# Performance work log

Measured on AMD Instinct MI355X. Metric: run time of the kernel, lower is better.

The kernel has to match this reference:

```python
import jax, jax.numpy as jnp
import numpy as np

N, E, R, H = 50000, 400000, 3, 3
IN, HID, OUT, C, B = 128, 64, 64, 16, 8


def _deg_norm(idx):
    # DGL GraphConv norm='both': deg.clamp(min=1) ** -0.5
    deg = jax.ops.segment_sum(jnp.ones(idx.shape, jnp.float32), idx, N)
    return jnp.maximum(deg, 1.0) ** -0.5


def _graph_conv(h, W, b, s, d):
    # h: [N, ..., F_in]; norm by src out-degree, matmul, scatter-sum to dst, norm by dst in-degree
    ns, nd = _deg_norm(s), _deg_norm(d)
    bshape = (N,) + (1,) * (h.ndim - 1)
    hw = (h * ns.reshape(bshape)) @ W
    agg = jax.ops.segment_sum(hw[s], d, N)
    return agg * nd.reshape(bshape) + b


def _gat(h, W, al, ar, b, s, d):
    # h: [N, HID] -> [N, H, HID] multi-head GAT with edge softmax over incoming edges
    f = (h @ W).reshape(N, H, HID)
    el = jnp.sum(f * al, axis=-1)  # [N, H]
    er = jnp.sum(f * ar, axis=-1)  # [N, H]
    e = jax.nn.leaky_relu(el[s] + er[d], 0.2)  # [E, H]
    m = jax.ops.segment_max(e, d, N)
    ez = jnp.exp(e - m[d])
    z = jax.ops.segment_sum(ez, d, N)
    alpha = ez / (z[d] + 1e-9)  # [E, H]
    out = jax.ops.segment_sum(alpha[:, :, None] * f[s], d, N)  # [N, H, HID]
    return out + b.reshape(H, HID)


def setup_inputs() -> dict:
    key = jax.random.key(0)
    k = jax.random.split(key, 12)
    s = 0.05
    return {
        "x": jax.random.normal(k[0], (N, IN), jnp.float32),
        "src": jax.random.randint(k[1], (R, E), 0, N, jnp.int32),
        "dst": jax.random.randint(k[2], (R, E), 0, N, jnp.int32),
        "graph_id": (jnp.arange(N, dtype=jnp.int32) * B // N).astype(jnp.int32),
        "W1": jax.random.normal(k[3], (R, IN, HID), jnp.float32) * s,
        "b1": jnp.zeros((R, HID), jnp.float32),
        "Wg": jax.random.normal(k[4], (R, HID, H * HID), jnp.float32) * s,
        "al": jax.random.normal(k[5], (R, H, HID), jnp.float32) * s,
        "ar": jax.random.normal(k[6], (R, H, HID), jnp.float32) * s,
        "bg": jnp.zeros((R, H * HID), jnp.float32),
        "W2": jax.random.normal(k[7], (R, HID, OUT), jnp.float32) * s,
        "b2": jnp.zeros((R, OUT), jnp.float32),
        "Wc": jax.random.normal(k[8], (OUT, C), jnp.float32) * s,
        "bc": jnp.zeros((C,), jnp.float32),
    }


def reference(x, src, dst, graph_id, W1, b1, Wg, al, ar, bg, W2, b2, Wc, bc):
    # conv1: per-relation GraphConv, aggregate='sum'
    h = sum(_graph_conv(x, W1[r], b1[r], src[r], dst[r]) for r in range(R))  # [N, HID]
    # F.normalize (L2 over dim=1, eps=1e-12)
    h = h / jnp.maximum(jnp.linalg.norm(h, axis=1, keepdims=True), 1e-12)
    # gatconv: per-relation GAT (3 heads), aggregate='sum'
    h = sum(_gat(h, Wg[r], al[r], ar[r], bg[r], src[r], dst[r]) for r in range(R))  # [N, H, HID]
    h = jax.nn.relu(h)
    # dropout(0.3) omitted: deterministic eval reference
    # conv2: GraphConv applied per head
    h = sum(_graph_conv(h, W2[r], b2[r], src[r], dst[r]) for r in range(R))  # [N, H, OUT]
    h = jax.nn.sigmoid(h)
    # dgl.mean_nodes over batched graphs
    cnt = jax.ops.segment_sum(jnp.ones((N,), jnp.float32), graph_id, B)
    pooled = jax.ops.segment_sum(h, graph_id, B) / jnp.maximum(cnt, 1.0)[:, None, None]  # [B, H, OUT]
    hg = jax.nn.sigmoid(pooled @ Wc + bc)  # [B, H, C]
    return jnp.mean(hg, axis=2)  # [B, H]
```

## Files before the change

kernel.cpp:

```cpp
#include <hip/hip_runtime.h>
#include <math.h>

#define NN 50000
#define EE 400000
#define RR 3
#define NH 3
#define FIN 128
#define HID 64
#define FOUT 64
#define NC 16
#define NB 8
#define NGAT 208

typedef __attribute__((ext_vector_type(8))) short v8s;
typedef __attribute__((ext_vector_type(4))) float v4f;
typedef unsigned short u16;
typedef __attribute__((ext_vector_type(4))) unsigned short u16x4;

__device__ __forceinline__ u16 f2b(float f) {
  unsigned u = __float_as_uint(f);
  return (u16)((u + 0x7fffu + ((u >> 16) & 1u)) >> 16);
}
__device__ __forceinline__ float b2f(u16 b) {
  return __uint_as_float(((unsigned)b) << 16);
}
__device__ __forceinline__ float wexp(float e) {
  e = e > 0.f ? e : 0.2f * e;
  return __expf(e);
}

__global__ void k_deg(const int* __restrict__ src, const int* __restrict__ dst,
                      int* __restrict__ degs, int* __restrict__ degd) {
  int i = blockIdx.x * 256 + threadIdx.x;
  if (i >= RR * EE) return;
  int r = i / EE;
  atomicAdd(&degs[r * NN + src[i]], 1);
  atomicAdd(&degd[r * NN + dst[i]], 1);
}

__global__ void k_norm(const int* __restrict__ degs, const int* __restrict__ degd,
                       float* __restrict__ ns, float* __restrict__ nd) {
  int i = blockIdx.x * 256 + threadIdx.x;
  if (i >= RR * NN) return;
  ns[i] = 1.0f / sqrtf((float)(degs[i] > 1 ? degs[i] : 1));
  nd[i] = 1.0f / sqrtf((float)(degd[i] > 1 ? degd[i] : 1));
}

__global__ void k_scan1(const int* __restrict__ deg, int* __restrict__ offs,
                        int* __restrict__ bsum) {
  __shared__ int sh[256];
  int gid = blockIdx.x * 256 + threadIdx.x;
  int v = (gid < RR * NN) ? deg[gid] : 0;
  sh[threadIdx.x] = v;
  __syncthreads();
  for (int off = 1; off < 256; off <<= 1) {
    int t = (threadIdx.x >= off) ? sh[threadIdx.x - off] : 0;
    __syncthreads();
    sh[threadIdx.x] += t;
    __syncthreads();
  }
  if (gid < RR * NN) offs[gid] = sh[threadIdx.x] - v;
  if (threadIdx.x == 255) bsum[blockIdx.x] = sh[255];
}

__global__ void k_scan2(int* __restrict__ bsum, int nb) {
  __shared__ int sh[1024];
  int v = (threadIdx.x < nb) ? bsum[threadIdx.x] : 0;
  sh[threadIdx.x] = v;
  __syncthreads();
  for (int off = 1; off < 1024; off <<= 1) {
    int t = (threadIdx.x >= off) ? sh[threadIdx.x - off] : 0;
    __syncthreads();
    sh[threadIdx.x] += t;
    __syncthreads();
  }
  if (threadIdx.x < nb) bsum[threadIdx.x] = sh[threadIdx.x] - v;
}

__global__ void k_scan3(int* __restrict__ offs, const int* __restrict__ bsum,
                        int* __restrict__ cursor) {
  int i = blockIdx.x * 256 + threadIdx.x;
  if (i >= RR * NN) return;
  int v = offs[i] + bsum[i / 256];
  offs[i] = v;
  cursor[i] = v;
}

__global__ void k_fill(const int* __restrict__ src, const int* __restrict__ dst,
                       int* __restrict__ cursor, int* __restrict__ esrc,
                       int* __restrict__ edst) {
  int i = blockIdx.x * 256 + threadIdx.x;
  if (i >= RR * EE) return;
  int r = i / EE;
  int d = dst[i];
  int pos = atomicAdd(&cursor[r * NN + d], 1);
  esrc[pos] = src[i];
  edst[pos] = d;
}

__global__ void k_cast(const float4* __restrict__ in, u16x4* __restrict__ out, int n4) {
  int i = blockIdx.x * 256 + threadIdx.x;
  if (i >= n4) return;
  float4 v = in[i];
  u16x4 o;
  o.x = f2b(v.x); o.y = f2b(v.y); o.z = f2b(v.z); o.w = f2b(v.w);
  out[i] = o;
}

__global__ void k_bcomp(const float* __restrict__ Wg, const float* __restrict__ al,
                        const float* __restrict__ ar, float* __restrict__ B) {
  int i = blockIdx.x * 256 + threadIdx.x;
  if (i >= RR * HID * NGAT) return;
  int col = i % NGAT;
  int k = (i / NGAT) % HID;
  int r = i / (NGAT * HID);
  float v = 0.f;
  if (col < NH * HID) {
    v = Wg[((size_t)(r * HID + k)) * (NH * HID) + col];
  } else if (col < NH * HID + 6) {
    int c2 = col - NH * HID;
    int isar = c2 / NH, h = c2 % NH;
    const float* wg = Wg + ((size_t)(r * HID + k)) * (NH * HID) + h * HID;
    const float* av = (isar ? ar : al) + (r * NH + h) * HID;
    float a = 0.f;
#pragma unroll 8
    for (int c = 0; c < HID; ++c) a += wg[c] * av[c];
    v = a;
  }
  B[i] = v;
}

template <int K, int N, int SCALE_MODE>
__global__ __launch_bounds__(256) void k_gemm(const u16* __restrict__ A,
                                              const float* __restrict__ B0, int bstr,
                                              u16* __restrict__ C0, long cstr,
                                              const float* __restrict__ s0, int sstr,
                                              int M) {
  constexpr int KP = K + 8;
  __shared__ __align__(16) u16 Bt[N * KP];
  const float* B = B0 + (size_t)blockIdx.y * bstr;
  u16* C = C0 + (size_t)blockIdx.y * cstr;
  const float* scale = s0 + (size_t)blockIdx.y * sstr;
  for (int i = threadIdx.x; i < K * N; i += 256) {
    int k = i / N, n = i % N;
    Bt[n * KP + k] = f2b(B[(size_t)k * N + n]);
  }
  __syncthreads();
  int wid = threadIdx.x >> 6, lane = threadIdx.x & 63;
  int l15 = lane & 15, lg = lane >> 4;
  constexpr int NT = N / 16;
  int ntiles = (M + 63) >> 6;
  for (int tile = blockIdx.x; tile < ntiles; tile += gridDim.x) {
    int mbase = tile * 64 + wid * 16;
    v4f acc[NT];
#pragma unroll
    for (int t = 0; t < NT; ++t) acc[t] = (v4f)(0.f);
    int arow = mbase + l15;
    if (arow >= M) arow = M - 1;
    const u16* ap = A + (size_t)arow * K + lg * 8;
#pragma unroll
    for (int ks = 0; ks < K / 32; ++ks) {
      v8s a = *(const v8s*)(ap + ks * 32);
#pragma unroll
      for (int t = 0; t < NT; ++t) {
        v8s b = *(const v8s*)(&Bt[(t * 16 + l15) * KP + lg * 8 + ks * 32]);
        acc[t] = __builtin_amdgcn_mfma_f32_16x16x32_bf16(a, b, acc[t], 0, 0, 0);
      }
    }
#pragma unroll
    for (int q = 0; q < 4; ++q) {
      int row = mbase + lg * 4 + q;
      if (row < M) {
        float s = 1.f;
        if (SCALE_MODE == 1) s = scale[row];
        if (SCALE_MODE == 2) s = scale[row / NH];
#pragma unroll
        for (int t = 0; t < NT; ++t)
          C[(size_t)row * N + t * 16 + l15] = f2b(acc[t][q] * s);
      }
    }
  }
}

__global__ void k_g1(const int* __restrict__ offs, const int* __restrict__ degd,
                     const int* __restrict__ esrc, const u16* __restrict__ hw,
                     const float* __restrict__ nd, const float* __restrict__ b1,
                     u16* __restrict__ h1b) {
  int node = blockIdx.x * 4 + (threadIdx.x >> 6);
  int lane = threadIdx.x & 63;
  if (node >= NN) return;
  float v = 0.f;
#pragma unroll
  for (int r = 0; r < RR; ++r) {
    int start = offs[r * NN + node];
    int deg = degd[r * NN + node];
    const u16* base = hw + (size_t)r * NN * HID + lane;
    float t = 0.f;
    int j = 0;
    for (; j + 4 <= deg; j += 4) {
      int s0 = esrc[start + j], s1 = esrc[start + j + 1];
      int s2 = esrc[start + j + 2], s3 = esrc[start + j + 3];
      float a0 = b2f(base[(size_t)s0 * HID]);
      float a1 = b2f(base[(size_t)s1 * HID]);
      float a2 = b2f(base[(size_t)s2 * HID]);
      float a3 = b2f(base[(size_t)s3 * HID]);
      t += (a0 + a1) + (a2 + a3);
    }
    for (; j < deg; ++j) t += b2f(base[(size_t)esrc[start + j] * HID]);
    v += t * nd[r * NN + node];
  }
  v += b1[lane] + b1[HID + lane] + b1[2 * HID + lane];
  float sq = v * v;
  for (int off = 32; off; off >>= 1) sq += __shfl_xor(sq, off);
  float nrm = sqrtf(sq);
  nrm = nrm > 1e-12f ? nrm : 1e-12f;
  h1b[node * HID + lane] = f2b(v / nrm);
}

__global__ void k_elx(const u16* __restrict__ fb, u16* __restrict__ elr) {
  int i = blockIdx.x * 256 + threadIdx.x;
  if (i >= RR * NN) return;
  const u16* row = fb + (size_t)i * NGAT + NH * HID;
  u16x4 a, b;
  a.x = row[0]; a.y = row[1]; a.z = row[2]; a.w = 0;
  b.x = row[3]; b.y = row[4]; b.z = row[5]; b.w = 0;
  *(u16x4*)(elr + (size_t)i * 8) = a;
  *(u16x4*)(elr + (size_t)i * 8 + 4) = b;
}

__global__ void k_ew(const int* __restrict__ esrc, const int* __restrict__ edst,
                     const u16* __restrict__ elr, u16* __restrict__ ew) {
  int i = blockIdx.x * 256 + threadIdx.x;
  if (i >= RR * EE) return;
  int r = i / EE;
  int s = esrc[i], d = edst[i];
  const u16* es = elr + ((size_t)(r * NN + s)) * 8;
  const u16* ed = elr + ((size_t)(r * NN + d)) * 8 + 4;
  u16x4 o;
  o.x = f2b(wexp(b2f(es[0]) + b2f(ed[0])));
  o.y = f2b(wexp(b2f(es[1]) + b2f(ed[1])));
  o.z = f2b(wexp(b2f(es[2]) + b2f(ed[2])));
  o.w = 0;
  *(u16x4*)(ew + (size_t)i * 4) = o;
}

__global__ void k_gatg(const int* __restrict__ offs, const int* __restrict__ degd,
                       const int* __restrict__ esrc, const u16* __restrict__ fb,
                       const u16* __restrict__ ew, const float* __restrict__ bg,
                       u16* __restrict__ gatb) {
  int node = blockIdx.x * 4 + (threadIdx.x >> 6);
  int lane = threadIdx.x & 63;
  if (node >= NN) return;
  float o0 = 0.f, o1 = 0.f, o2 = 0.f;
#pragma unroll
  for (int r = 0; r < RR; ++r) {
    const u16* f = fb + (size_t)r * NN * NGAT + lane;
    int start = offs[r * NN + node];
    int deg = degd[r * NN + node];
    float z0 = 0.f, z1 = 0.f, z2 = 0.f;
    float a0 = 0.f, a1 = 0.f, a2 = 0.f;
    int j = 0;
    for (; j + 4 <= deg; j += 4) {
      int p = start + j;
      int s0 = esrc[p], s1 = esrc[p + 1], s2 = esrc[p + 2], s3 = esrc[p + 3];
      u16x4 wa = *(const u16x4*)(ew + (size_t)p * 4);
      u16x4 wb = *(const u16x4*)(ew + (size_t)(p + 1) * 4);
      u16x4 wc = *(const u16x4*)(ew + (size_t)(p + 2) * 4);
      u16x4 wd = *(const u16x4*)(ew + (size_t)(p + 3) * 4);
      const u16* q0 = f + (size_t)s0 * NGAT;
      const u16* q1 = f + (size_t)s1 * NGAT;
      const u16* q2 = f + (size_t)s2 * NGAT;
      const u16* q3 = f + (size_t)s3 * NGAT;
      float w;
      w = b2f(wa.x); z0 += w; a0 += w * b2f(q0[0]);
      w = b2f(wa.y); z1 += w; a1 += w * b2f(q0[HID]);
      w = b2f(wa.z); z2 += w; a2 += w * b2f(q0[2 * HID]);
      w = b2f(wb.x); z0 += w; a0 += w * b2f(q1[0]);
      w = b2f(wb.y); z1 += w; a1 += w * b2f(q1[HID]);
      w = b2f(wb.z); z2 += w; a2 += w * b2f(q1[2 * HID]);
      w = b2f(wc.x); z0 += w; a0 += w * b2f(q2[0]);
      w = b2f(wc.y); z1 += w; a1 += w * b2f(q2[HID]);
      w = b2f(wc.z); z2 += w; a2 += w * b2f(q2[2 * HID]);
      w = b2f(wd.x); z0 += w; a0 += w * b2f(q3[0]);
      w = b2f(wd.y); z1 += w; a1 += w * b2f(q3[HID]);
      w = b2f(wd.z); z2 += w; a2 += w * b2f(q3[2 * HID]);
    }
    for (; j < deg; ++j) {
      int p = start + j;
      int s0 = esrc[p];
      u16x4 wa = *(const u16x4*)(ew + (size_t)p * 4);
      const u16* q0 = f + (size_t)s0 * NGAT;
      float w;
      w = b2f(wa.x); z0 += w; a0 += w * b2f(q0[0]);
      w = b2f(wa.y); z1 += w; a1 += w * b2f(q0[HID]);
      w = b2f(wa.z); z2 += w; a2 += w * b2f(q0[2 * HID]);
    }
    o0 += a0 / (z0 + 1e-9f);
    o1 += a1 / (z1 + 1e-9f);
    o2 += a2 / (z2 + 1e-9f);
  }
  float ov[NH] = {o0, o1, o2};
#pragma unroll
  for (int h = 0; h < NH; ++h) {
    int j = h * HID + lane;
    float v = ov[h] + bg[j] + bg[NH * HID + j] + bg[2 * NH * HID + j];
    gatb[(size_t)node * (NH * HID) + j] = f2b(fmaxf(v, 0.f));
  }
}

__global__ void k_g2(const int* __restrict__ offs, const int* __restrict__ degd,
                     const int* __restrict__ esrc, const u16* __restrict__ fb,
                     const float* __restrict__ nd, const float* __restrict__ b2,
                     u16* __restrict__ agg2b) {
  int node = blockIdx.x * 4 + (threadIdx.x >> 6);
  int lane = threadIdx.x & 63;
  if (node >= NN) return;
  float o0 = 0.f, o1 = 0.f, o2 = 0.f;
#pragma unroll
  for (int r = 0; r < RR; ++r) {
    const u16* hw = fb + (size_t)r * NN * NH * FOUT + lane;
    int start = offs[r * NN + node];
    int deg = degd[r * NN + node];
    float a0 = 0.f, a1 = 0.f, a2 = 0.f;
    int j = 0;
    for (; j + 4 <= deg; j += 4) {
      int p = start + j;
      const u16* q0 = hw + (size_t)esrc[p] * (NH * FOUT);
      const u16* q1 = hw + (size_t)esrc[p + 1] * (NH * FOUT);
      const u16* q2 = hw + (size_t)esrc[p + 2] * (NH * FOUT);
      const u16* q3 = hw + (size_t)esrc[p + 3] * (NH * FOUT);
      a0 += (b2f(q0[0]) + b2f(q1[0])) + (b2f(q2[0]) + b2f(q3[0]));
      a1 += (b2f(q0[FOUT]) + b2f(q1[FOUT])) + (b2f(q2[FOUT]) + b2f(q3[FOUT]));
      a2 += (b2f(q0[2 * FOUT]) + b2f(q1[2 * FOUT])) +
            (b2f(q2[2 * FOUT]) + b2f(q3[2 * FOUT]));
    }
    for (; j < deg; ++j) {
      const u16* q0 = hw + (size_t)esrc[start + j] * (NH * FOUT);
      a0 += b2f(q0[0]);
      a1 += b2f(q0[FOUT]);
      a2 += b2f(q0[2 * FOUT]);
    }
    float ndv = nd[r * NN + node];
    o0 += a0 * ndv; o1 += a1 * ndv; o2 += a2 * ndv;
  }
  float b2s = b2[lane] + b2[FOUT + lane] + b2[2 * FOUT + lane];
  float ov[NH] = {o0, o1, o2};
#pragma unroll
  for (int h = 0; h < NH; ++h) {
    float v = 1.0f / (1.0f + __expf(-(ov[h] + b2s)));
    agg2b[(size_t)node * (NH * FOUT) + h * FOUT + lane] = f2b(v);
  }
}

__global__ void k_cnt2(const int* __restrict__ gid, float* __restrict__ cnt) {
  __shared__ int loc[NB];
  if (threadIdx.x < NB) loc[threadIdx.x] = 0;
  __syncthreads();
  int i = blockIdx.x * 256 + threadIdx.x;
  if (i < NN) atomicAdd(&loc[gid[i]], 1);
  __syncthreads();
  if (threadIdx.x < NB) atomicAdd(&cnt[threadIdx.x], (float)loc[threadIdx.x]);
}

__global__ void k_pool(const u16* __restrict__ h3, const int* __restrict__ gid,
                       float* __restrict__ pooled) {
  int j = threadIdx.x;
  int start = blockIdx.x * 128;
  if (start >= NN) return;
  int end = start + 128;
  if (end > NN) end = NN;
  int gcur = gid[start];
  float acc = 0.f;
  for (int n = start; n < end; ++n) {
    int g = gid[n];
    if (g != gcur) {
      atomicAdd(&pooled[gcur * (NH * FOUT) + j], acc);
      acc = 0.f;
      gcur = g;
    }
    acc += b2f(h3[(size_t)n * (NH * FOUT) + j]);
  }
  atomicAdd(&pooled[gcur * (NH * FOUT) + j], acc);
}

__global__ void k_final(const float* __restrict__ pooled, const float* __restrict__ cnt,
                        const float* __restrict__ Wc, const float* __restrict__ bc,
                        float* __restrict__ out) {
  int t = threadIdx.x;
  if (t >= NB * NH) return;
  int b = t / NH;
  float inv = 1.0f / fmaxf(cnt[b], 1.0f);
  const float* p = pooled + t * FOUT;
  float sacc = 0.f;
  for (int c = 0; c < NC; ++c) {
    float acc = bc[c];
    for (int o = 0; o < FOUT; ++o) acc += p[o] * inv * Wc[o * NC + c];
    sacc += 1.0f / (1.0f + __expf(-acc));
  }
  out[t] = sacc * (1.0f / NC);
}

extern "C" void kernel_launch(void* const* d_in, const int* in_sizes, int n_in,
                              void* d_out, int out_size, void* d_ws, size_t ws_size,
                              hipStream_t stream) {
  const float* x = (const float*)d_in[0];
  const int* src = (const int*)d_in[1];
  const int* dst = (const int*)d_in[2];
  const int* gid = (const int*)d_in[3];
  const float* W1 = (const float*)d_in[4];
  const float* b1 = (const float*)d_in[5];
  const float* Wg = (const float*)d_in[6];
  const float* al = (const float*)d_in[7];
  const float* ar = (const float*)d_in[8];
  const float* bg = (const float*)d_in[9];
  const float* W2 = (const float*)d_in[10];
  const float* b2 = (const float*)d_in[11];
  const float* Wc = (const float*)d_in[12];
  const float* bc = (const float*)d_in[13];
  float* out = (float*)d_out;

  int* degs = (int*)d_ws;
  int* degd = degs + RR * NN;
  float* cnt = (float*)(degd + RR * NN);
  float* pooled = cnt + NB;
  size_t zero_bytes = ((size_t)2 * RR * NN + NB + NB * NH * FOUT) * 4;
  int* offs = (int*)(pooled + NB * NH * FOUT);
  int* cursor = offs + RR * NN + 8;
  int* bsum = cursor + RR * NN;
  int* esrc = bsum + 1024;
  int* edst = esrc + (size_t)RR * EE;
  float* ns = (float*)(edst + (size_t)RR * EE);
  float* nd = ns + RR * NN;
  float* Bcomp = nd + RR * NN;
  u16* elr = (u16*)(Bcomp + RR * HID * NGAT);
  u16* ew = elr + (size_t)RR * NN * 8;
  u16* xb = ew + (size_t)RR * EE * 4;
  u16* h1b = xb + (size_t)NN * FIN;
  u16* fb = h1b + (size_t)NN * HID;
  u16* gatb = fb + (size_t)RR * NN * NGAT;
  u16* agg2b = xb;

  hipMemsetAsync(d_ws, 0, zero_bytes, stream);

  const int nscan = RR * NN;
  const int nblk1 = (nscan + 255) / 256;

  k_deg<<<(RR * EE + 255) / 256, 256, 0, stream>>>(src, dst, degs, degd);
  k_norm<<<(nscan + 255) / 256, 256, 0, stream>>>(degs, degd, ns, nd);
  k_scan1<<<nblk1, 256, 0, stream>>>(degd, offs, bsum);
  k_scan2<<<1, 1024, 0, stream>>>(bsum, nblk1);
  k_scan3<<<nblk1, 256, 0, stream>>>(offs, bsum, cursor);
  k_fill<<<(RR * EE + 255) / 256, 256, 0, stream>>>(src, dst, cursor, esrc, edst);

  k_cast<<<(NN * FIN / 4 + 255) / 256, 256, 0, stream>>>((const float4*)x, (u16x4*)xb,
                                                         NN * FIN / 4);
  k_bcomp<<<(RR * HID * NGAT + 255) / 256, 256, 0, stream>>>(Wg, al, ar, Bcomp);

  k_gemm<FIN, HID, 1><<<dim3(782, RR), 256, 0, stream>>>(
      xb, W1, FIN * HID, fb, (long)NN * HID, ns, NN, NN);
  k_g1<<<(NN + 3) / 4, 256, 0, stream>>>(offs, degd, esrc, fb, nd, b1, h1b);

  k_gemm<HID, NGAT, 0><<<dim3(782, RR), 256, 0, stream>>>(
      h1b, Bcomp, HID * NGAT, fb, (long)NN * NGAT, ns, 0, NN);
  k_elx<<<(nscan + 255) / 256, 256, 0, stream>>>(fb, elr);
  k_ew<<<(RR * EE + 255) / 256, 256, 0, stream>>>(esrc, edst, elr, ew);
  k_gatg<<<(NN + 3) / 4, 256, 0, stream>>>(offs, degd, esrc, fb, ew, bg, gatb);

  k_gemm<HID, FOUT, 2><<<dim3(2344, RR), 256, 0, stream>>>(
      gatb, W2, HID * FOUT, fb, (long)NN * NH * FOUT, ns, NN, NN * NH);
  k_g2<<<(NN + 3) / 4, 256, 0, stream>>>(offs, degd, esrc, fb, nd, b2, agg2b);

  k_cnt2<<<(NN + 255) / 256, 256, 0, stream>>>(gid, cnt);
  k_pool<<<(NN + 127) / 128, 192, 0, stream>>>(agg2b, gid, pooled);
  k_final<<<1, 64, 0, stream>>>(pooled, cnt, Wc, bc, out);
}
```

Baseline: 686.2 us.

## Store gathered GEMM outputs as scaled fp8, packed per head for one-word gathers

```diff
diff --git a/kernel.cpp b/kernel.cpp
--- a/kernel.cpp
+++ b/kernel.cpp
@@ -15,7 +15,12 @@
 typedef __attribute__((ext_vector_type(8))) short v8s;
 typedef __attribute__((ext_vector_type(4))) float v4f;
 typedef unsigned short u16;
+typedef unsigned char u8;
+typedef unsigned int u32;
 typedef __attribute__((ext_vector_type(4))) unsigned short u16x4;
+
+#define QS 32.0f
+#define IQS (1.0f / 32.0f)
 
 __device__ __forceinline__ u16 f2b(float f) {
   unsigned u = __float_as_uint(f);
@@ -27,6 +32,9 @@
 __device__ __forceinline__ float wexp(float e) {
   e = e > 0.f ? e : 0.2f * e;
   return __expf(e);
+}
+__device__ __forceinline__ u8 f2e(float v) {
+  return (u8)(__builtin_amdgcn_cvt_pk_fp8_f32(v, 0.f, 0, false) & 0xff);
 }
 
 __global__ void k_deg(const int* __restrict__ src, const int* __restrict__ dst,
@@ -130,17 +138,20 @@
   B[i] = v;
 }
 
-template <int K, int N, int SCALE_MODE>
-__global__ __launch_bounds__(256) void k_gemm(const u16* __restrict__ A,
+template <int K, int N, int OUTMODE>
+__global__ __launch_bounds__(256) void k_gemm(const u16* __restrict__ A, int lda,
                                               const float* __restrict__ B0, int bstr,
-                                              u16* __restrict__ C0, long cstr,
-                                              const float* __restrict__ s0, int sstr,
-                                              int M) {
+                                              void* __restrict__ C0,
+                                              u16* __restrict__ elr,
+                                              const float* __restrict__ s0, int M) {
   constexpr int KP = K + 8;
   __shared__ __align__(16) u16 Bt[N * KP];
-  const float* B = B0 + (size_t)blockIdx.y * bstr;
-  u16* C = C0 + (size_t)blockIdx.y * cstr;
-  const float* scale = s0 + (size_t)blockIdx.y * sstr;
+  int y = blockIdx.y;
+  int rrel = (OUTMODE == 3) ? y / NH : y;
+  int head = (OUTMODE == 3) ? y % NH : 0;
+  const float* B = B0 + (size_t)rrel * bstr;
+  const float* scale = s0 + (size_t)rrel * NN;
+  const u16* Ab = A + head * HID;
   for (int i = threadIdx.x; i < K * N; i += 256) {
     int k = i / N, n = i % N;
     Bt[n * KP + k] = f2b(B[(size_t)k * N + n]);
@@ -157,7 +168,7 @@
     for (int t = 0; t < NT; ++t) acc[t] = (v4f)(0.f);
     int arow = mbase + l15;
     if (arow >= M) arow = M - 1;
-    const u16* ap = A + (size_t)arow * K + lg * 8;
+    const u16* ap = Ab + (size_t)arow * lda + lg * 8;
 #pragma unroll
     for (int ks = 0; ks < K / 32; ++ks) {
       v8s a = *(const v8s*)(ap + ks * 32);
@@ -170,20 +181,36 @@
 #pragma unroll
     for (int q = 0; q < 4; ++q) {
       int row = mbase + lg * 4 + q;
-      if (row < M) {
-        float s = 1.f;
-        if (SCALE_MODE == 1) s = scale[row];
-        if (SCALE_MODE == 2) s = scale[row / NH];
-#pragma unroll
-        for (int t = 0; t < NT; ++t)
-          C[(size_t)row * N + t * 16 + l15] = f2b(acc[t][q] * s);
+      if (row >= M) continue;
+      if (OUTMODE == 1) {
+        float s = scale[row] * QS;
+        u8* C = (u8*)C0 + ((size_t)y * M + row) * 64;
+#pragma unroll
+        for (int t = 0; t < NT; ++t) C[t * 16 + l15] = f2e(acc[t][q] * s);
+      } else if (OUTMODE == 2) {
+        u32* C = (u32*)C0 + ((size_t)y * M + row) * 64;
+#pragma unroll
+        for (int tm = 0; tm < 4; ++tm) {
+          u32 pk = __builtin_amdgcn_cvt_pk_fp8_f32(acc[tm][q] * QS,
+                                                   acc[tm + 4][q] * QS, 0, false);
+          pk = __builtin_amdgcn_cvt_pk_fp8_f32(acc[tm + 8][q] * QS, 0.f, pk, true);
+          C[tm * 16 + l15] = pk;
+        }
+        if (l15 < 6)
+          elr[((size_t)y * M + row) * 8 + (l15 < 3 ? l15 : l15 + 1)] =
+              f2b(acc[12][q]);
+      } else {
+        float s = scale[row] * QS;
+        u8* C = (u8*)C0 + (((size_t)rrel * M + row) * 64) * 4 + head;
+#pragma unroll
+        for (int t = 0; t < NT; ++t) C[(t * 16 + l15) * 4] = f2e(acc[t][q] * s);
       }
     }
   }
 }
 
 __global__ void k_g1(const int* __restrict__ offs, const int* __restrict__ degd,
-                     const int* __restrict__ esrc, const u16* __restrict__ hw,
+                     const int* __restrict__ esrc, const u8* __restrict__ c1pk,
                      const float* __restrict__ nd, const float* __restrict__ b1,
                      u16* __restrict__ h1b) {
   int node = blockIdx.x * 4 + (threadIdx.x >> 6);
@@ -194,38 +221,28 @@
   for (int r = 0; r < RR; ++r) {
     int start = offs[r * NN + node];
     int deg = degd[r * NN + node];
-    const u16* base = hw + (size_t)r * NN * HID + lane;
+    const u8* base = c1pk + (size_t)r * NN * 64 + lane;
     float t = 0.f;
     int j = 0;
     for (; j + 4 <= deg; j += 4) {
       int s0 = esrc[start + j], s1 = esrc[start + j + 1];
       int s2 = esrc[start + j + 2], s3 = esrc[start + j + 3];
-      float a0 = b2f(base[(size_t)s0 * HID]);
-      float a1 = b2f(base[(size_t)s1 * HID]);
-      float a2 = b2f(base[(size_t)s2 * HID]);
-      float a3 = b2f(base[(size_t)s3 * HID]);
+      float a0 = __builtin_amdgcn_cvt_f32_fp8((u32)base[(size_t)s0 * 64], 0);
+      float a1 = __builtin_amdgcn_cvt_f32_fp8((u32)base[(size_t)s1 * 64], 0);
+      float a2 = __builtin_amdgcn_cvt_f32_fp8((u32)base[(size_t)s2 * 64], 0);
+      float a3 = __builtin_amdgcn_cvt_f32_fp8((u32)base[(size_t)s3 * 64], 0);
       t += (a0 + a1) + (a2 + a3);
     }
-    for (; j < deg; ++j) t += b2f(base[(size_t)esrc[start + j] * HID]);
+    for (; j < deg; ++j)
+      t += __builtin_amdgcn_cvt_f32_fp8((u32)base[(size_t)esrc[start + j] * 64], 0);
     v += t * nd[r * NN + node];
   }
-  v += b1[lane] + b1[HID + lane] + b1[2 * HID + lane];
+  v = v * IQS + b1[lane] + b1[HID + lane] + b1[2 * HID + lane];
   float sq = v * v;
   for (int off = 32; off; off >>= 1) sq += __shfl_xor(sq, off);
   float nrm = sqrtf(sq);
   nrm = nrm > 1e-12f ? nrm : 1e-12f;
   h1b[node * HID + lane] = f2b(v / nrm);
-}
-
-__global__ void k_elx(const u16* __restrict__ fb, u16* __restrict__ elr) {
-  int i = blockIdx.x * 256 + threadIdx.x;
-  if (i >= RR * NN) return;
-  const u16* row = fb + (size_t)i * NGAT + NH * HID;
-  u16x4 a, b;
-  a.x = row[0]; a.y = row[1]; a.z = row[2]; a.w = 0;
-  b.x = row[3]; b.y = row[4]; b.z = row[5]; b.w = 0;
-  *(u16x4*)(elr + (size_t)i * 8) = a;
-  *(u16x4*)(elr + (size_t)i * 8 + 4) = b;
 }
 
 __global__ void k_ew(const int* __restrict__ esrc, const int* __restrict__ edst,
@@ -245,7 +262,7 @@
 }
 
 __global__ void k_gatg(const int* __restrict__ offs, const int* __restrict__ degd,
-                       const int* __restrict__ esrc, const u16* __restrict__ fb,
+                       const int* __restrict__ esrc, const u32* __restrict__ fpk,
                        const u16* __restrict__ ew, const float* __restrict__ bg,
                        u16* __restrict__ gatb) {
   int node = blockIdx.x * 4 + (threadIdx.x >> 6);
@@ -254,7 +271,7 @@
   float o0 = 0.f, o1 = 0.f, o2 = 0.f;
 #pragma unroll
   for (int r = 0; r < RR; ++r) {
-    const u16* f = fb + (size_t)r * NN * NGAT + lane;
+    const u32* f = fpk + (size_t)r * NN * 64 + lane;
     int start = offs[r * NN + node];
     int deg = degd[r * NN + node];
     float z0 = 0.f, z1 = 0.f, z2 = 0.f;
@@ -267,33 +284,32 @@
       u16x4 wb = *(const u16x4*)(ew + (size_t)(p + 1) * 4);
       u16x4 wc = *(const u16x4*)(ew + (size_t)(p + 2) * 4);
       u16x4 wd = *(const u16x4*)(ew + (size_t)(p + 3) * 4);
-      const u16* q0 = f + (size_t)s0 * NGAT;
-      const u16* q1 = f + (size_t)s1 * NGAT;
-      const u16* q2 = f + (size_t)s2 * NGAT;
-      const u16* q3 = f + (size_t)s3 * NGAT;
+      u32 v0 = f[(size_t)s0 * 64];
+      u32 v1 = f[(size_t)s1 * 64];
+      u32 v2 = f[(size_t)s2 * 64];
+      u32 v3 = f[(size_t)s3 * 64];
       float w;
-      w = b2f(wa.x); z0 += w; a0 += w * b2f(q0[0]);
-      w = b2f(wa.y); z1 += w; a1 += w * b2f(q0[HID]);
-      w = b2f(wa.z); z2 += w; a2 += w * b2f(q0[2 * HID]);
-      w = b2f(wb.x); z0 += w; a0 += w * b2f(q1[0]);
-      w = b2f(wb.y); z1 += w; a1 += w * b2f(q1[HID]);
-      w = b2f(wb.z); z2 += w; a2 += w * b2f(q1[2 * HID]);
-      w = b2f(wc.x); z0 += w; a0 += w * b2f(q2[0]);
-      w = b2f(wc.y); z1 += w; a1 += w * b2f(q2[HID]);
-      w = b2f(wc.z); z2 += w; a2 += w * b2f(q2[2 * HID]);
-      w = b2f(wd.x); z0 += w; a0 += w * b2f(q3[0]);
-      w = b2f(wd.y); z1 += w; a1 += w * b2f(q3[HID]);
-      w = b2f(wd.z); z2 += w; a2 += w * b2f(q3[2 * HID]);
+      w = b2f(wa.x); z0 += w; a0 += w * __builtin_amdgcn_cvt_f32_fp8(v0, 0);
+      w = b2f(wa.y); z1 += w; a1 += w * __builtin_amdgcn_cvt_f32_fp8(v0, 1);
+      w = b2f(wa.z); z2 += w; a2 += w * __builtin_amdgcn_cvt_f32_fp8(v0, 2);
+      w = b2f(wb.x); z0 += w; a0 += w * __builtin_amdgcn_cvt_f32_fp8(v1, 0);
+      w = b2f(wb.y); z1 += w; a1 += w * __builtin_amdgcn_cvt_f32_fp8(v1, 1);
+      w = b2f(wb.z); z2 += w; a2 += w * __builtin_amdgcn_cvt_f32_fp8(v1, 2);
+      w = b2f(wc.x); z0 += w; a0 += w * __builtin_amdgcn_cvt_f32_fp8(v2, 0);
+      w = b2f(wc.y); z1 += w; a1 += w * __builtin_amdgcn_cvt_f32_fp8(v2, 1);
+      w = b2f(wc.z); z2 += w; a2 += w * __builtin_amdgcn_cvt_f32_fp8(v2, 2);
+      w = b2f(wd.x); z0 += w; a0 += w * __builtin_amdgcn_cvt_f32_fp8(v3, 0);
+      w = b2f(wd.y); z1 += w; a1 += w * __builtin_amdgcn_cvt_f32_fp8(v3, 1);
+      w = b2f(wd.z); z2 += w; a2 += w * __builtin_amdgcn_cvt_f32_fp8(v3, 2);
     }
     for (; j < deg; ++j) {
       int p = start + j;
-      int s0 = esrc[p];
       u16x4 wa = *(const u16x4*)(ew + (size_t)p * 4);
-      const u16* q0 = f + (size_t)s0 * NGAT;
+      u32 v0 = f[(size_t)esrc[p] * 64];
       float w;
-      w = b2f(wa.x); z0 += w; a0 += w * b2f(q0[0]);
-      w = b2f(wa.y); z1 += w; a1 += w * b2f(q0[HID]);
-      w = b2f(wa.z); z2 += w; a2 += w * b2f(q0[2 * HID]);
+      w = b2f(wa.x); z0 += w; a0 += w * __builtin_amdgcn_cvt_f32_fp8(v0, 0);
+      w = b2f(wa.y); z1 += w; a1 += w * __builtin_amdgcn_cvt_f32_fp8(v0, 1);
+      w = b2f(wa.z); z2 += w; a2 += w * __builtin_amdgcn_cvt_f32_fp8(v0, 2);
     }
     o0 += a0 / (z0 + 1e-9f);
     o1 += a1 / (z1 + 1e-9f);
@@ -303,13 +319,13 @@
 #pragma unroll
   for (int h = 0; h < NH; ++h) {
     int j = h * HID + lane;
-    float v = ov[h] + bg[j] + bg[NH * HID + j] + bg[2 * NH * HID + j];
+    float v = ov[h] * IQS + bg[j] + bg[NH * HID + j] + bg[2 * NH * HID + j];
     gatb[(size_t)node * (NH * HID) + j] = f2b(fmaxf(v, 0.f));
   }
 }
 
 __global__ void k_g2(const int* __restrict__ offs, const int* __restrict__ degd,
-                     const int* __restrict__ esrc, const u16* __restrict__ fb,
+                     const int* __restrict__ esrc, const u32* __restrict__ c2pk,
                      const float* __restrict__ nd, const float* __restrict__ b2,
                      u16* __restrict__ agg2b) {
   int node = blockIdx.x * 4 + (threadIdx.x >> 6);
@@ -318,27 +334,29 @@
   float o0 = 0.f, o1 = 0.f, o2 = 0.f;
 #pragma unroll
   for (int r = 0; r < RR; ++r) {
-    const u16* hw = fb + (size_t)r * NN * NH * FOUT + lane;
+    const u32* hw = c2pk + (size_t)r * NN * 64 + lane;
     int start = offs[r * NN + node];
     int deg = degd[r * NN + node];
     float a0 = 0.f, a1 = 0.f, a2 = 0.f;
     int j = 0;
     for (; j + 4 <= deg; j += 4) {
       int p = start + j;
-      const u16* q0 = hw + (size_t)esrc[p] * (NH * FOUT);
-      const u16* q1 = hw + (size_t)esrc[p + 1] * (NH * FOUT);
-      const u16* q2 = hw + (size_t)esrc[p + 2] * (NH * FOUT);
-      const u16* q3 = hw + (size_t)esrc[p + 3] * (NH * FOUT);
-      a0 += (b2f(q0[0]) + b2f(q1[0])) + (b2f(q2[0]) + b2f(q3[0]));
-      a1 += (b2f(q0[FOUT]) + b2f(q1[FOUT])) + (b2f(q2[FOUT]) + b2f(q3[FOUT]));
-      a2 += (b2f(q0[2 * FOUT]) + b2f(q1[2 * FOUT])) +
-            (b2f(q2[2 * FOUT]) + b2f(q3[2 * FOUT]));
+      u32 v0 = hw[(size_t)esrc[p] * 64];
+      u32 v1 = hw[(size_t)esrc[p + 1] * 64];
+      u32 v2 = hw[(size_t)esrc[p + 2] * 64];
+      u32 v3 = hw[(size_t)esrc[p + 3] * 64];
+      a0 += (__builtin_amdgcn_cvt_f32_fp8(v0, 0) + __builtin_amdgcn_cvt_f32_fp8(v1, 0)) +
+            (__builtin_amdgcn_cvt_f32_fp8(v2, 0) + __builtin_amdgcn_cvt_f32_fp8(v3, 0));
+      a1 += (__builtin_amdgcn_cvt_f32_fp8(v0, 1) + __builtin_amdgcn_cvt_f32_fp8(v1, 1)) +
+            (__builtin_amdgcn_cvt_f32_fp8(v2, 1) + __builtin_amdgcn_cvt_f32_fp8(v3, 1));
+      a2 += (__builtin_amdgcn_cvt_f32_fp8(v0, 2) + __builtin_amdgcn_cvt_f32_fp8(v1, 2)) +
+            (__builtin_amdgcn_cvt_f32_fp8(v2, 2) + __builtin_amdgcn_cvt_f32_fp8(v3, 2));
     }
     for (; j < deg; ++j) {
-      const u16* q0 = hw + (size_t)esrc[start + j] * (NH * FOUT);
-      a0 += b2f(q0[0]);
-      a1 += b2f(q0[FOUT]);
-      a2 += b2f(q0[2 * FOUT]);
+      u32 v0 = hw[(size_t)esrc[start + j] * 64];
+      a0 += __builtin_amdgcn_cvt_f32_fp8(v0, 0);
+      a1 += __builtin_amdgcn_cvt_f32_fp8(v0, 1);
+      a2 += __builtin_amdgcn_cvt_f32_fp8(v0, 2);
     }
     float ndv = nd[r * NN + node];
     o0 += a0 * ndv; o1 += a1 * ndv; o2 += a2 * ndv;
@@ -347,7 +365,7 @@
   float ov[NH] = {o0, o1, o2};
 #pragma unroll
   for (int h = 0; h < NH; ++h) {
-    float v = 1.0f / (1.0f + __expf(-(ov[h] + b2s)));
+    float v = 1.0f / (1.0f + __expf(-(ov[h] * IQS + b2s)));
     agg2b[(size_t)node * (NH * FOUT) + h * FOUT + lane] = f2b(v);
   }
 }
@@ -436,8 +454,10 @@
   u16* ew = elr + (size_t)RR * NN * 8;
   u16* xb = ew + (size_t)RR * EE * 4;
   u16* h1b = xb + (size_t)NN * FIN;
-  u16* fb = h1b + (size_t)NN * HID;
-  u16* gatb = fb + (size_t)RR * NN * NGAT;
+  u8* c1pk = (u8*)(h1b + (size_t)NN * HID);
+  u16* gatb = (u16*)(c1pk + (size_t)RR * NN * 64);
+  u32* fpk = (u32*)(gatb + (size_t)NN * NH * HID);
+  u32* c2pk = fpk;
   u16* agg2b = xb;
 
   hipMemsetAsync(d_ws, 0, zero_bytes, stream);
@@ -457,18 +477,17 @@
   k_bcomp<<<(RR * HID * NGAT + 255) / 256, 256, 0, stream>>>(Wg, al, ar, Bcomp);
 
   k_gemm<FIN, HID, 1><<<dim3(782, RR), 256, 0, stream>>>(
-      xb, W1, FIN * HID, fb, (long)NN * HID, ns, NN, NN);
-  k_g1<<<(NN + 3) / 4, 256, 0, stream>>>(offs, degd, esrc, fb, nd, b1, h1b);
-
-  k_gemm<HID, NGAT, 0><<<dim3(782, RR), 256, 0, stream>>>(
-      h1b, Bcomp, HID * NGAT, fb, (long)NN * NGAT, ns, 0, NN);
-  k_elx<<<(nscan + 255) / 256, 256, 0, stream>>>(fb, elr);
+      xb, FIN, W1, FIN * HID, c1pk, nullptr, ns, NN);
+  k_g1<<<(NN + 3) / 4, 256, 0, stream>>>(offs, degd, esrc, c1pk, nd, b1, h1b);
+
+  k_gemm<HID, NGAT, 2><<<dim3(782, RR), 256, 0, stream>>>(
+      h1b, HID, Bcomp, HID * NGAT, fpk, elr, ns, NN);
   k_ew<<<(RR * EE + 255) / 256, 256, 0, stream>>>(esrc, edst, elr, ew);
-  k_gatg<<<(NN + 3) / 4, 256, 0, stream>>>(offs, degd, esrc, fb, ew, bg, gatb);
-
-  k_gemm<HID, FOUT, 2><<<dim3(2344, RR), 256, 0, stream>>>(
-      gatb, W2, HID * FOUT, fb, (long)NN * NH * FOUT, ns, NN, NN * NH);
-  k_g2<<<(NN + 3) / 4, 256, 0, stream>>>(offs, degd, esrc, fb, nd, b2, agg2b);
+  k_gatg<<<(NN + 3) / 4, 256, 0, stream>>>(offs, degd, esrc, fpk, ew, bg, gatb);
+
+  k_gemm<HID, FOUT, 3><<<dim3(782, RR * NH), 256, 0, stream>>>(
+      gatb, NH * HID, W2, HID * FOUT, c2pk, nullptr, ns, NN);
+  k_g2<<<(NN + 3) / 4, 256, 0, stream>>>(offs, degd, esrc, c2pk, nd, b2, agg2b);
 
   k_cnt2<<<(NN + 255) / 256, 256, 0, stream>>>(gid, cnt);
   k_pool<<<(NN + 127) / 128, 192, 0, stream>>>(agg2b, gid, pooled);
```

After: 666.9 us. 2.8% less time.
